# Performance work log

Measured on AMD Instinct MI355X. Metric: run time of the kernel, lower is better.

## Reference

```python
import jax, jax.numpy as jnp
import numpy as np

N_NODES = 50000
N_EDGES = 800000
IN_CH = 128
HID = 128
LAT = 64


def setup_inputs() -> dict:
    key = jax.random.key(0)
    ks = jax.random.split(key, 8)
    s = 1.0 / np.sqrt(IN_CH)
    sh = 1.0 / np.sqrt(HID)
    x = jax.random.normal(ks[0], (N_NODES, IN_CH), dtype=jnp.float32)
    edge_index = jax.random.randint(ks[1], (2, N_EDGES), 0, N_NODES, dtype=jnp.int64)
    return {
        "x": x,
        "edge_index": edge_index,
        "W1": jax.random.normal(ks[2], (IN_CH, HID), dtype=jnp.float32) * s,
        "b1": jnp.zeros((HID,), dtype=jnp.float32),
        "W2": jax.random.normal(ks[3], (HID, HID), dtype=jnp.float32) * sh,
        "b2": jnp.zeros((HID,), dtype=jnp.float32),
        "W_mu": jax.random.normal(ks[4], (HID, LAT), dtype=jnp.float32) * sh,
        "b_mu": jnp.zeros((LAT,), dtype=jnp.float32),
        "W_lv": jax.random.normal(ks[5], (HID, LAT), dtype=jnp.float32) * sh,
        "b_lv": jnp.zeros((LAT,), dtype=jnp.float32),
    }


def _gcn_norm(edge_index, num_nodes):
    # PyG gcn_norm with add_self_loops=True: deg[i] = in-degree(i) + 1
    src, dst = edge_index[0], edge_index[1]
    deg = jax.ops.segment_sum(jnp.ones((edge_index.shape[1],), jnp.float32), dst,
                              num_segments=num_nodes) + 1.0
    dinv = 1.0 / jnp.sqrt(deg)  # deg >= 1, never inf
    edge_norm = dinv[src] * dinv[dst]          # [E]
    self_norm = dinv * dinv                    # [N] norm for self-loop edges
    return src, dst, edge_norm, self_norm


def _gcn_conv(x, W, b, src, dst, edge_norm, self_norm, num_nodes):
    h = x @ W                                           # [N, out]
    msg = h[src] * edge_norm[:, None]                   # [E, out] gather
    agg = jax.ops.segment_sum(msg, dst, num_segments=num_nodes)  # scatter-add
    agg = agg + h * self_norm[:, None]                  # self-loop contribution
    return agg + b


def reference(x, edge_index, W1, b1, W2, b2, W_mu, b_mu, W_lv, b_lv):
    n = x.shape[0]
    src, dst, e_norm, s_norm = _gcn_norm(edge_index, n)
    h = jax.nn.relu(_gcn_conv(x, W1, b1, src, dst, e_norm, s_norm, n))
    h = jax.nn.relu(_gcn_conv(h, W2, b2, src, dst, e_norm, s_norm, n))
    mu = h @ W_mu + b_mu
    logvar = h @ W_lv + b_lv
    return mu, logvar
```

## Files before the change

### kernel.cpp

```cpp
#include <hip/hip_runtime.h>

#define NN 50000
#define NE 800000
#define NSLICE 6250
#define BKT 64

typedef short s8v  __attribute__((ext_vector_type(8)));
typedef float f4v  __attribute__((ext_vector_type(4)));

__device__ __forceinline__ unsigned f2bf(float f) {
    unsigned u = __float_as_uint(f);
    return (u + 0x7fffu + ((u >> 16) & 1u)) >> 16;
}
__device__ __forceinline__ float bf2f_lo(unsigned u) { return __uint_as_float(u << 16); }
__device__ __forceinline__ float bf2f_hi(unsigned u) { return __uint_as_float(u & 0xffff0000u); }

__device__ __forceinline__ s8v pack8(float4 p, float4 q) {
    union { unsigned u[4]; s8v v; } r;
    r.u[0] = (f2bf(p.y) << 16) | f2bf(p.x);
    r.u[1] = (f2bf(p.w) << 16) | f2bf(p.z);
    r.u[2] = (f2bf(q.y) << 16) | f2bf(q.x);
    r.u[3] = (f2bf(q.w) << 16) | f2bf(q.z);
    return r.v;
}

__global__ __launch_bounds__(256) void k_prep(const float* __restrict__ W1, const float* __restrict__ W2,
                                              const float* __restrict__ Wmu, const float* __restrict__ Wlv,
                                              unsigned short* __restrict__ Wt, int* __restrict__ cursor) {
    int b = blockIdx.x;
    if (b < 192) {
        int idx = b * 256 + threadIdx.x;
        int m = idx >> 14, i = idx & 16383;
        int n = i & 127, k = i >> 7;
        float v;
        if (m == 0)      v = W1[k * 128 + n];
        else if (m == 1) v = W2[k * 128 + n];
        else             v = (n < 64) ? Wmu[k * 64 + n] : Wlv[k * 64 + (n - 64)];
        Wt[m * 16384 + n * 128 + k] = (unsigned short)f2bf(v);
    } else {
        int i = (b - 192) * 256 + threadIdx.x;
        if (i < NN) cursor[i] = 0;
    }
}

__global__ __launch_bounds__(256) void k_fg(const float4* __restrict__ x4,
                                            const unsigned short* __restrict__ Wt,
                                            unsigned short* __restrict__ Hb,
                                            const int* __restrict__ src, const int* __restrict__ dst,
                                            int* __restrict__ cursor, int* __restrict__ esrc) {
    int b = blockIdx.x;
    if (b < 782) {
        int wave = threadIdx.x >> 6, lane = threadIdx.x & 63;
        int quad = lane >> 4, l16 = lane & 15;
        int row0 = b * 64 + wave * 16;
        int arow = row0 + l16;
        int arc  = arow < NN ? arow : NN - 1;

        const float4* xq = x4 + (size_t)arc * 32;
        s8v a0 = pack8(xq[ 0 + quad * 2], xq[ 1 + quad * 2]);
        s8v a1 = pack8(xq[ 8 + quad * 2], xq[ 9 + quad * 2]);
        s8v a2 = pack8(xq[16 + quad * 2], xq[17 + quad * 2]);
        s8v a3 = pack8(xq[24 + quad * 2], xq[25 + quad * 2]);

        f4v acc[8];
#pragma unroll
        for (int c = 0; c < 8; ++c) acc[c] = (f4v)0.f;

#pragma unroll
        for (int c = 0; c < 8; ++c) {
            const s8v* wp = (const s8v*)(Wt + (size_t)(c * 16 + l16) * 128);
            acc[c] = __builtin_amdgcn_mfma_f32_16x16x32_bf16(a0, wp[quad],      acc[c], 0, 0, 0);
            acc[c] = __builtin_amdgcn_mfma_f32_16x16x32_bf16(a1, wp[4 + quad],  acc[c], 0, 0, 0);
            acc[c] = __builtin_amdgcn_mfma_f32_16x16x32_bf16(a2, wp[8 + quad],  acc[c], 0, 0, 0);
            acc[c] = __builtin_amdgcn_mfma_f32_16x16x32_bf16(a3, wp[12 + quad], acc[c], 0, 0, 0);
        }

#pragma unroll
        for (int c = 0; c < 8; ++c) {
#pragma unroll
            for (int r = 0; r < 4; ++r) {
                int ro = row0 + quad * 4 + r;
                if (ro < NN) Hb[(size_t)ro * 128 + c * 16 + l16] = (unsigned short)f2bf(acc[c][r]);
            }
        }
    } else {
        int bb = b - 782;
        int xcd = b & 7;
        int e = (bb >> 3) * 256 + threadIdx.x;
        if (e >= NE) return;
        int d = dst[e];
        if (d / NSLICE != xcd) return;
        int s = src[e];
        int p = atomicAdd(&cursor[d], 1);
        if (p < BKT) esrc[(size_t)d * BKT + p] = s;
    }
}

__global__ __launch_bounds__(256) void k_gemm(const unsigned short* __restrict__ Xb,
                                              const unsigned short* __restrict__ Wt,
                                              unsigned short* __restrict__ Cb, int N) {
    int wave = threadIdx.x >> 6, lane = threadIdx.x & 63;
    int quad = lane >> 4, l16 = lane & 15;
    int row0 = blockIdx.x * 64 + wave * 16;
    int arow = row0 + l16;
    int arc  = arow < N ? arow : N - 1;

    const s8v* xp = (const s8v*)(Xb + (size_t)arc * 128);
    s8v a0 = xp[quad], a1 = xp[4 + quad], a2 = xp[8 + quad], a3 = xp[12 + quad];

    f4v acc[8];
#pragma unroll
    for (int c = 0; c < 8; ++c) acc[c] = (f4v)0.f;

#pragma unroll
    for (int c = 0; c < 8; ++c) {
        const s8v* wp = (const s8v*)(Wt + (size_t)(c * 16 + l16) * 128);
        acc[c] = __builtin_amdgcn_mfma_f32_16x16x32_bf16(a0, wp[quad],      acc[c], 0, 0, 0);
        acc[c] = __builtin_amdgcn_mfma_f32_16x16x32_bf16(a1, wp[4 + quad],  acc[c], 0, 0, 0);
        acc[c] = __builtin_amdgcn_mfma_f32_16x16x32_bf16(a2, wp[8 + quad],  acc[c], 0, 0, 0);
        acc[c] = __builtin_amdgcn_mfma_f32_16x16x32_bf16(a3, wp[12 + quad], acc[c], 0, 0, 0);
    }

#pragma unroll
    for (int c = 0; c < 8; ++c) {
#pragma unroll
        for (int r = 0; r < 4; ++r) {
            int ro = row0 + quad * 4 + r;
            if (ro < N) Cb[(size_t)ro * 128 + c * 16 + l16] = (unsigned short)f2bf(acc[c][r]);
        }
    }
}

__global__ __launch_bounds__(256) void k_final(const unsigned short* __restrict__ Xb,
                                               const unsigned short* __restrict__ Wt,
                                               const float* __restrict__ bmu, const float* __restrict__ blv,
                                               float* __restrict__ out, int N) {
    int wave = threadIdx.x >> 6, lane = threadIdx.x & 63;
    int quad = lane >> 4, l16 = lane & 15;
    int row0 = blockIdx.x * 64 + wave * 16;
    int arow = row0 + l16;
    int arc  = arow < N ? arow : N - 1;

    const s8v* xp = (const s8v*)(Xb + (size_t)arc * 128);
    s8v a0 = xp[quad], a1 = xp[4 + quad], a2 = xp[8 + quad], a3 = xp[12 + quad];

    f4v acc[8];
#pragma unroll
    for (int c = 0; c < 8; ++c) acc[c] = (f4v)0.f;

#pragma unroll
    for (int c = 0; c < 8; ++c) {
        const s8v* wp = (const s8v*)(Wt + (size_t)(c * 16 + l16) * 128);
        acc[c] = __builtin_amdgcn_mfma_f32_16x16x32_bf16(a0, wp[quad],      acc[c], 0, 0, 0);
        acc[c] = __builtin_amdgcn_mfma_f32_16x16x32_bf16(a1, wp[4 + quad],  acc[c], 0, 0, 0);
        acc[c] = __builtin_amdgcn_mfma_f32_16x16x32_bf16(a2, wp[8 + quad],  acc[c], 0, 0, 0);
        acc[c] = __builtin_amdgcn_mfma_f32_16x16x32_bf16(a3, wp[12 + quad], acc[c], 0, 0, 0);
    }

#pragma unroll
    for (int c = 0; c < 8; ++c) {
        int col  = c * 16 + l16;
        float bb = (col < 64) ? bmu[col] : blv[col - 64];
#pragma unroll
        for (int r = 0; r < 4; ++r) {
            int ro = row0 + quad * 4 + r;
            if (ro < N) {
                float v = acc[c][r] + bb;
                if (col < 64) out[(size_t)ro * 64 + col] = v;
                else          out[(size_t)NN * 64 + (size_t)ro * 64 + (col - 64)] = v;
            }
        }
    }
}

template<bool FIRST>
__global__ __launch_bounds__(256) void k_agg(const unsigned short* __restrict__ hb,
                                             const int* __restrict__ degc,
                                             const int* __restrict__ esrc,
                                             float* __restrict__ dinv,
                                             const float* __restrict__ b,
                                             unsigned short* __restrict__ outb) {
    int lane = threadIdx.x & 63;
    int n = blockIdx.x * 4 + (threadIdx.x >> 6);
    int d = __builtin_amdgcn_readfirstlane(degc[n]);
    float dn;
    if (FIRST) {
        dn = rsqrtf((float)(d + 1));
        if (lane == 0) dinv[n] = dn;
    } else {
        dn = __uint_as_float(__builtin_amdgcn_readfirstlane(__float_as_uint(dinv[n])));
    }
    const unsigned* h2 = (const unsigned*)hb;
    const int* bk = esrc + (size_t)n * BKT;
    int sv = bk[lane];

    float ax0 = 0.f, ay0 = 0.f, ax1 = 0.f, ay1 = 0.f;
    float ax2 = 0.f, ay2 = 0.f, ax3 = 0.f, ay3 = 0.f;

    {
        unsigned u[24];
        float    w[24];
#pragma unroll
        for (int k = 0; k < 24; ++k) {
            int sraw = __builtin_amdgcn_readlane(sv, k);
            unsigned su = ((unsigned)sraw < (unsigned)NN) ? (unsigned)sraw : 0u;
            float ws;
            if (FIRST) {
                int cs = __builtin_amdgcn_readfirstlane(degc[su]);
                ws = rsqrtf((float)(cs + 1));
            } else {
                ws = __uint_as_float(__builtin_amdgcn_readfirstlane(__float_as_uint(dinv[su])));
            }
            w[k] = (k < d) ? ws * dn : 0.f;
            u[k] = h2[(size_t)su * 64 + lane];
        }
#pragma unroll
        for (int k = 0; k < 24; ++k) {
            float lo = bf2f_lo(u[k]), hi = bf2f_hi(u[k]);
            switch (k & 3) {
                case 0: ax0 += lo * w[k]; ay0 += hi * w[k]; break;
                case 1: ax1 += lo * w[k]; ay1 += hi * w[k]; break;
                case 2: ax2 += lo * w[k]; ay2 += hi * w[k]; break;
                default: ax3 += lo * w[k]; ay3 += hi * w[k]; break;
            }
        }
    }

    for (int e0 = 24; e0 < d; e0 += 8) {
        unsigned u[8];
        float    w[8];
#pragma unroll
        for (int k = 0; k < 8; ++k) {
            int ek  = e0 + k;
            int ekc = ek < (BKT - 1) ? ek : (BKT - 1);
            int sraw = __builtin_amdgcn_readlane(sv, ekc);
            unsigned su = ((unsigned)sraw < (unsigned)NN) ? (unsigned)sraw : 0u;
            float ws;
            if (FIRST) {
                int cs = __builtin_amdgcn_readfirstlane(degc[su]);
                ws = rsqrtf((float)(cs + 1));
            } else {
                ws = __uint_as_float(__builtin_amdgcn_readfirstlane(__float_as_uint(dinv[su])));
            }
            w[k] = (ek < d) ? ws * dn : 0.f;
            u[k] = h2[(size_t)su * 64 + lane];
        }
#pragma unroll
        for (int k = 0; k < 8; ++k) {
            float lo = bf2f_lo(u[k]), hi = bf2f_hi(u[k]);
            switch (k & 3) {
                case 0: ax0 += lo * w[k]; ay0 += hi * w[k]; break;
                case 1: ax1 += lo * w[k]; ay1 += hi * w[k]; break;
                case 2: ax2 += lo * w[k]; ay2 += hi * w[k]; break;
                default: ax3 += lo * w[k]; ay3 += hi * w[k]; break;
            }
        }
    }

    float sn = dn * dn;
    unsigned uh = h2[(size_t)n * 64 + lane];
    float2 bb = ((const float2*)b)[lane];
    float rx = fmaxf((ax0 + ax1) + (ax2 + ax3) + bf2f_lo(uh) * sn + bb.x, 0.f);
    float ry = fmaxf((ay0 + ay1) + (ay2 + ay3) + bf2f_hi(uh) * sn + bb.y, 0.f);
    ((unsigned*)outb)[(size_t)n * 64 + lane] = (f2bf(ry) << 16) | f2bf(rx);
}

extern "C" void kernel_launch(void* const* d_in, const int* in_sizes, int n_in,
                              void* d_out, int out_size, void* d_ws, size_t ws_size,
                              hipStream_t stream) {
    const float* x    = (const float*)d_in[0];
    const int*   eidx = (const int*)d_in[1];
    const float* W1   = (const float*)d_in[2];
    const float* b1   = (const float*)d_in[3];
    const float* W2   = (const float*)d_in[4];
    const float* b2   = (const float*)d_in[5];
    const float* Wmu  = (const float*)d_in[6];
    const float* bmu  = (const float*)d_in[7];
    const float* Wlv  = (const float*)d_in[8];
    const float* blv  = (const float*)d_in[9];
    float* out = (float*)d_out;

    const int* src = eidx;
    const int* dst = eidx + NE;

    float*          ws     = (float*)d_ws;
    int*            cursor = (int*)ws;
    float*          dinv   = ws + 50048;
    int*            esrc   = (int*)(ws + 100096);
    unsigned short* Wt     = (unsigned short*)(ws + 3300096);
    unsigned short* Hb     = (unsigned short*)(ws + 3324672);
    unsigned short* Gb     = (unsigned short*)(ws + 6524672);

    const int gFG = 782 + ((NE + 255) / 256) * 8;
    const int gG  = (NN + 63) / 64;
    const int gA  = NN / 4;

    k_prep<<<388, 256, 0, stream>>>(W1, W2, Wmu, Wlv, Wt, cursor);

    k_fg<<<gFG, 256, 0, stream>>>((const float4*)x, Wt, Hb, src, dst, cursor, esrc);

    k_agg<true><<<gA, 256, 0, stream>>>(Hb, cursor, esrc, dinv, b1, Gb);

    k_gemm<<<gG, 256, 0, stream>>>(Gb, Wt + 16384, Hb, NN);
    k_agg<false><<<gA, 256, 0, stream>>>(Hb, cursor, esrc, dinv, b2, Gb);

    k_final<<<gG, 256, 0, stream>>>(Gb, Wt + 32768, bmu, blv, out, NN);
}
```

Baseline: 270.8 us.

## Fuse aggregation with following GEMM via LDS and vectorize edge bucketing

Merges each aggregation kernel with the next GEMM: every wave aggregates 16 node rows into a swizzled LDS tile, then runs MFMA on it directly, which removes two launches and the bf16 round trip of the aggregated features through global memory. The edge-bucketing part now reads four edges per thread with int4 loads and is placed before the GEMM blocks in the grid. In exchange, each aggregation wave handles 16 rows serially, so fewer independent waves are in flight to hide the random gather latency.

After: 293.8 us. +8.5%, slower.

```diff
diff --git a/kernel.cpp b/kernel.cpp
--- a/kernel.cpp
+++ b/kernel.cpp
@@ -49,10 +49,27 @@
                                             const int* __restrict__ src, const int* __restrict__ dst,
                                             int* __restrict__ cursor, int* __restrict__ esrc) {
     int b = blockIdx.x;
-    if (b < 782) {
+    if (b < 6256) {
+        int xcd = b & 7;
+        int idx = (b >> 3) * 256 + (int)threadIdx.x;
+        if (idx >= NE / 4) return;
+        int4 d4 = ((const int4*)dst)[idx];
+        int4 s4 = ((const int4*)src)[idx];
+        int dv[4] = { d4.x, d4.y, d4.z, d4.w };
+        int sv[4] = { s4.x, s4.y, s4.z, s4.w };
+#pragma unroll
+        for (int k = 0; k < 4; ++k) {
+            int d = dv[k];
+            if (d / NSLICE == xcd) {
+                int p = atomicAdd(&cursor[d], 1);
+                if (p < BKT) esrc[(size_t)d * BKT + p] = sv[k];
+            }
+        }
+    } else {
+        int bg = b - 6256;
         int wave = threadIdx.x >> 6, lane = threadIdx.x & 63;
         int quad = lane >> 4, l16 = lane & 15;
-        int row0 = b * 64 + wave * 16;
+        int row0 = bg * 64 + wave * 16;
         int arow = row0 + l16;
         int arc  = arow < NN ? arow : NN - 1;
 
@@ -83,116 +100,25 @@
                 if (ro < NN) Hb[(size_t)ro * 128 + c * 16 + l16] = (unsigned short)f2bf(acc[c][r]);
             }
         }
-    } else {
-        int bb = b - 782;
-        int xcd = b & 7;
-        int e = (bb >> 3) * 256 + threadIdx.x;
-        if (e >= NE) return;
-        int d = dst[e];
-        if (d / NSLICE != xcd) return;
-        int s = src[e];
-        int p = atomicAdd(&cursor[d], 1);
-        if (p < BKT) esrc[(size_t)d * BKT + p] = s;
-    }
-}
-
-__global__ __launch_bounds__(256) void k_gemm(const unsigned short* __restrict__ Xb,
-                                              const unsigned short* __restrict__ Wt,
-                                              unsigned short* __restrict__ Cb, int N) {
-    int wave = threadIdx.x >> 6, lane = threadIdx.x & 63;
-    int quad = lane >> 4, l16 = lane & 15;
-    int row0 = blockIdx.x * 64 + wave * 16;
-    int arow = row0 + l16;
-    int arc  = arow < N ? arow : N - 1;
-
-    const s8v* xp = (const s8v*)(Xb + (size_t)arc * 128);
-    s8v a0 = xp[quad], a1 = xp[4 + quad], a2 = xp[8 + quad], a3 = xp[12 + quad];
-
-    f4v acc[8];
-#pragma unroll
-    for (int c = 0; c < 8; ++c) acc[c] = (f4v)0.f;
-
-#pragma unroll
-    for (int c = 0; c < 8; ++c) {
-        const s8v* wp = (const s8v*)(Wt + (size_t)(c * 16 + l16) * 128);
-        acc[c] = __builtin_amdgcn_mfma_f32_16x16x32_bf16(a0, wp[quad],      acc[c], 0, 0, 0);
-        acc[c] = __builtin_amdgcn_mfma_f32_16x16x32_bf16(a1, wp[4 + quad],  acc[c], 0, 0, 0);
-        acc[c] = __builtin_amdgcn_mfma_f32_16x16x32_bf16(a2, wp[8 + quad],  acc[c], 0, 0, 0);
-        acc[c] = __builtin_amdgcn_mfma_f32_16x16x32_bf16(a3, wp[12 + quad], acc[c], 0, 0, 0);
-    }
-
-#pragma unroll
-    for (int c = 0; c < 8; ++c) {
-#pragma unroll
-        for (int r = 0; r < 4; ++r) {
-            int ro = row0 + quad * 4 + r;
-            if (ro < N) Cb[(size_t)ro * 128 + c * 16 + l16] = (unsigned short)f2bf(acc[c][r]);
-        }
-    }
-}
-
-__global__ __launch_bounds__(256) void k_final(const unsigned short* __restrict__ Xb,
-                                               const unsigned short* __restrict__ Wt,
-                                               const float* __restrict__ bmu, const float* __restrict__ blv,
-                                               float* __restrict__ out, int N) {
-    int wave = threadIdx.x >> 6, lane = threadIdx.x & 63;
-    int quad = lane >> 4, l16 = lane & 15;
-    int row0 = blockIdx.x * 64 + wave * 16;
-    int arow = row0 + l16;
-    int arc  = arow < N ? arow : N - 1;
-
-    const s8v* xp = (const s8v*)(Xb + (size_t)arc * 128);
-    s8v a0 = xp[quad], a1 = xp[4 + quad], a2 = xp[8 + quad], a3 = xp[12 + quad];
-
-    f4v acc[8];
-#pragma unroll
-    for (int c = 0; c < 8; ++c) acc[c] = (f4v)0.f;
-
-#pragma unroll
-    for (int c = 0; c < 8; ++c) {
-        const s8v* wp = (const s8v*)(Wt + (size_t)(c * 16 + l16) * 128);
-        acc[c] = __builtin_amdgcn_mfma_f32_16x16x32_bf16(a0, wp[quad],      acc[c], 0, 0, 0);
-        acc[c] = __builtin_amdgcn_mfma_f32_16x16x32_bf16(a1, wp[4 + quad],  acc[c], 0, 0, 0);
-        acc[c] = __builtin_amdgcn_mfma_f32_16x16x32_bf16(a2, wp[8 + quad],  acc[c], 0, 0, 0);
-        acc[c] = __builtin_amdgcn_mfma_f32_16x16x32_bf16(a3, wp[12 + quad], acc[c], 0, 0, 0);
-    }
-
-#pragma unroll
-    for (int c = 0; c < 8; ++c) {
-        int col  = c * 16 + l16;
-        float bb = (col < 64) ? bmu[col] : blv[col - 64];
-#pragma unroll
-        for (int r = 0; r < 4; ++r) {
-            int ro = row0 + quad * 4 + r;
-            if (ro < N) {
-                float v = acc[c][r] + bb;
-                if (col < 64) out[(size_t)ro * 64 + col] = v;
-                else          out[(size_t)NN * 64 + (size_t)ro * 64 + (col - 64)] = v;
-            }
-        }
     }
 }
 
 template<bool FIRST>
-__global__ __launch_bounds__(256) void k_agg(const unsigned short* __restrict__ hb,
-                                             const int* __restrict__ degc,
-                                             const int* __restrict__ esrc,
-                                             float* __restrict__ dinv,
-                                             const float* __restrict__ b,
-                                             unsigned short* __restrict__ outb) {
-    int lane = threadIdx.x & 63;
-    int n = blockIdx.x * 4 + (threadIdx.x >> 6);
-    int d = __builtin_amdgcn_readfirstlane(degc[n]);
+__device__ __forceinline__ float2 agg_row(const unsigned* __restrict__ h2,
+                                          const int* __restrict__ degc,
+                                          const int* __restrict__ esrc,
+                                          float* __restrict__ dinv,
+                                          const float* __restrict__ b,
+                                          int nc, int lane) {
+    int d = __builtin_amdgcn_readfirstlane(degc[nc]);
     float dn;
     if (FIRST) {
         dn = rsqrtf((float)(d + 1));
-        if (lane == 0) dinv[n] = dn;
+        if (lane == 0) dinv[nc] = dn;
     } else {
-        dn = __uint_as_float(__builtin_amdgcn_readfirstlane(__float_as_uint(dinv[n])));
-    }
-    const unsigned* h2 = (const unsigned*)hb;
-    const int* bk = esrc + (size_t)n * BKT;
-    int sv = bk[lane];
+        dn = __uint_as_float(__builtin_amdgcn_readfirstlane(__float_as_uint(dinv[nc])));
+    }
+    int sv = esrc[(size_t)nc * BKT + lane];
 
     float ax0 = 0.f, ay0 = 0.f, ax1 = 0.f, ay1 = 0.f;
     float ax2 = 0.f, ay2 = 0.f, ax3 = 0.f, ay3 = 0.f;
@@ -258,11 +184,119 @@
     }
 
     float sn = dn * dn;
-    unsigned uh = h2[(size_t)n * 64 + lane];
+    unsigned uh = h2[(size_t)nc * 64 + lane];
     float2 bb = ((const float2*)b)[lane];
-    float rx = fmaxf((ax0 + ax1) + (ax2 + ax3) + bf2f_lo(uh) * sn + bb.x, 0.f);
-    float ry = fmaxf((ay0 + ay1) + (ay2 + ay3) + bf2f_hi(uh) * sn + bb.y, 0.f);
-    ((unsigned*)outb)[(size_t)n * 64 + lane] = (f2bf(ry) << 16) | f2bf(rx);
+    float2 r;
+    r.x = fmaxf((ax0 + ax1) + (ax2 + ax3) + bf2f_lo(uh) * sn + bb.x, 0.f);
+    r.y = fmaxf((ay0 + ay1) + (ay2 + ay3) + bf2f_hi(uh) * sn + bb.y, 0.f);
+    return r;
+}
+
+__global__ __launch_bounds__(256) void k_ag(const unsigned short* __restrict__ Hb_,
+                                            const int* __restrict__ degc, const int* __restrict__ esrc,
+                                            float* __restrict__ dinv, const float* __restrict__ b1,
+                                            const unsigned short* __restrict__ Wt,
+                                            unsigned short* __restrict__ Cb) {
+    __shared__ __align__(16) unsigned lds[4][16][64];
+    int wave = threadIdx.x >> 6, lane = threadIdx.x & 63;
+    int quad = lane >> 4, l16 = lane & 15;
+    int row0 = blockIdx.x * 64 + wave * 16;
+    const unsigned* h2 = (const unsigned*)Hb_;
+
+#pragma unroll 1
+    for (int j = 0; j < 16; ++j) {
+        int n = row0 + j;
+        int nc = n < NN ? n : NN - 1;
+        float2 r = agg_row<true>(h2, degc, esrc, dinv, b1, nc, lane);
+        lds[wave][j][lane ^ ((j & 7) << 2)] = (f2bf(r.y) << 16) | f2bf(r.x);
+    }
+    __syncthreads();
+
+    const unsigned* rowp = &lds[wave][l16][0];
+    int kx = l16 & 7;
+    s8v a0 = *(const s8v*)(rowp + (( 0 + quad) ^ kx) * 4);
+    s8v a1 = *(const s8v*)(rowp + (( 4 + quad) ^ kx) * 4);
+    s8v a2 = *(const s8v*)(rowp + (( 8 + quad) ^ kx) * 4);
+    s8v a3 = *(const s8v*)(rowp + ((12 + quad) ^ kx) * 4);
+
+    f4v acc[8];
+#pragma unroll
+    for (int c = 0; c < 8; ++c) acc[c] = (f4v)0.f;
+
+#pragma unroll
+    for (int c = 0; c < 8; ++c) {
+        const s8v* wp = (const s8v*)(Wt + (size_t)(c * 16 + l16) * 128);
+        acc[c] = __builtin_amdgcn_mfma_f32_16x16x32_bf16(a0, wp[quad],      acc[c], 0, 0, 0);
+        acc[c] = __builtin_amdgcn_mfma_f32_16x16x32_bf16(a1, wp[4 + quad],  acc[c], 0, 0, 0);
+        acc[c] = __builtin_amdgcn_mfma_f32_16x16x32_bf16(a2, wp[8 + quad],  acc[c], 0, 0, 0);
+        acc[c] = __builtin_amdgcn_mfma_f32_16x16x32_bf16(a3, wp[12 + quad], acc[c], 0, 0, 0);
+    }
+
+#pragma unroll
+    for (int c = 0; c < 8; ++c) {
+#pragma unroll
+        for (int r = 0; r < 4; ++r) {
+            int ro = row0 + quad * 4 + r;
+            if (ro < NN) Cb[(size_t)ro * 128 + c * 16 + l16] = (unsigned short)f2bf(acc[c][r]);
+        }
+    }
+}
+
+__global__ __launch_bounds__(256) void k_af(const unsigned short* __restrict__ Hb_,
+                                            const int* __restrict__ degc, const int* __restrict__ esrc,
+                                            float* __restrict__ dinv, const float* __restrict__ b2,
+                                            const unsigned short* __restrict__ Wt,
+                                            const float* __restrict__ bmu, const float* __restrict__ blv,
+                                            float* __restrict__ out) {
+    __shared__ __align__(16) unsigned lds[4][16][64];
+    int wave = threadIdx.x >> 6, lane = threadIdx.x & 63;
+    int quad = lane >> 4, l16 = lane & 15;
+    int row0 = blockIdx.x * 64 + wave * 16;
+    const unsigned* h2 = (const unsigned*)Hb_;
+
+#pragma unroll 1
+    for (int j = 0; j < 16; ++j) {
+        int n = row0 + j;
+        int nc = n < NN ? n : NN - 1;
+        float2 r = agg_row<false>(h2, degc, esrc, dinv, b2, nc, lane);
+        lds[wave][j][lane ^ ((j & 7) << 2)] = (f2bf(r.y) << 16) | f2bf(r.x);
+    }
+    __syncthreads();
+
+    const unsigned* rowp = &lds[wave][l16][0];
+    int kx = l16 & 7;
+    s8v a0 = *(const s8v*)(rowp + (( 0 + quad) ^ kx) * 4);
+    s8v a1 = *(const s8v*)(rowp + (( 4 + quad) ^ kx) * 4);
+    s8v a2 = *(const s8v*)(rowp + (( 8 + quad) ^ kx) * 4);
+    s8v a3 = *(const s8v*)(rowp + ((12 + quad) ^ kx) * 4);
+
+    f4v acc[8];
+#pragma unroll
+    for (int c = 0; c < 8; ++c) acc[c] = (f4v)0.f;
+
+#pragma unroll
+    for (int c = 0; c < 8; ++c) {
+        const s8v* wp = (const s8v*)(Wt + (size_t)(c * 16 + l16) * 128);
+        acc[c] = __builtin_amdgcn_mfma_f32_16x16x32_bf16(a0, wp[quad],      acc[c], 0, 0, 0);
+        acc[c] = __builtin_amdgcn_mfma_f32_16x16x32_bf16(a1, wp[4 + quad],  acc[c], 0, 0, 0);
+        acc[c] = __builtin_amdgcn_mfma_f32_16x16x32_bf16(a2, wp[8 + quad],  acc[c], 0, 0, 0);
+        acc[c] = __builtin_amdgcn_mfma_f32_16x16x32_bf16(a3, wp[12 + quad], acc[c], 0, 0, 0);
+    }
+
+#pragma unroll
+    for (int c = 0; c < 8; ++c) {
+        int col  = c * 16 + l16;
+        float bb = (col < 64) ? bmu[col] : blv[col - 64];
+#pragma unroll
+        for (int r = 0; r < 4; ++r) {
+            int ro = row0 + quad * 4 + r;
+            if (ro < NN) {
+                float v = acc[c][r] + bb;
+                if (col < 64) out[(size_t)ro * 64 + col] = v;
+                else          out[(size_t)NN * 64 + (size_t)ro * 64 + (col - 64)] = v;
+            }
+        }
+    }
 }
 
 extern "C" void kernel_launch(void* const* d_in, const int* in_sizes, int n_in,
@@ -289,20 +323,16 @@
     int*            esrc   = (int*)(ws + 100096);
     unsigned short* Wt     = (unsigned short*)(ws + 3300096);
     unsigned short* Hb     = (unsigned short*)(ws + 3324672);
-    unsigned short* Gb     = (unsigned short*)(ws + 6524672);
-
-    const int gFG = 782 + ((NE + 255) / 256) * 8;
-    const int gG  = (NN + 63) / 64;
-    const int gA  = NN / 4;
+    unsigned short* Hb2    = (unsigned short*)(ws + 6524672);
+
+    const int gFG = 6256 + 782;
+    const int gA  = 782;
 
     k_prep<<<388, 256, 0, stream>>>(W1, W2, Wmu, Wlv, Wt, cursor);
 
     k_fg<<<gFG, 256, 0, stream>>>((const float4*)x, Wt, Hb, src, dst, cursor, esrc);
 
-    k_agg<true><<<gA, 256, 0, stream>>>(Hb, cursor, esrc, dinv, b1, Gb);
-
-    k_gemm<<<gG, 256, 0, stream>>>(Gb, Wt + 16384, Hb, NN);
-    k_agg<false><<<gA, 256, 0, stream>>>(Hb, cursor, esrc, dinv, b2, Gb);
-
-    k_final<<<gG, 256, 0, stream>>>(Gb, Wt + 32768, bmu, blv, out, NN);
-}
+    k_ag<<<gA, 256, 0, stream>>>(Hb, cursor, esrc, dinv, b1, Wt + 16384, Hb2);
+
+    k_af<<<gA, 256, 0, stream>>>(Hb2, cursor, esrc, dinv, b2, Wt + 32768, bmu, blv, out);
+}
```

## Drop XCD-sliced edge bucketing, put scatter blocks first, use nontemporal stores

Applied to the files above, without the earlier changes.

The edge-bucketing part of the fused GEMM/bucket kernel no longer launches 8 block copies per edge chunk, each filtering edges by destination slice tied to its XCD. It now uses one block per 256 edges with no filtering. Those blocks are scheduled before the GEMM blocks so the atomic scatter starts earlier. The change cuts redundant reads of src/dst and wasted blocks, but loses the L2 locality the per-XCD slicing gave the cursor atomics. All intermediate and final output stores become nontemporal, to avoid polluting cache with streaming writes, though Hb/Gb are re-read by the next kernel.

Result: slower. 294.0 us (+8.6%).

```diff
diff --git a/kernel.cpp b/kernel.cpp
--- a/kernel.cpp
+++ b/kernel.cpp
@@ -2,7 +2,6 @@
 
 #define NN 50000
 #define NE 800000
-#define NSLICE 6250
 #define BKT 64
 
 typedef short s8v  __attribute__((ext_vector_type(8)));
@@ -49,10 +48,17 @@
                                             const int* __restrict__ src, const int* __restrict__ dst,
                                             int* __restrict__ cursor, int* __restrict__ esrc) {
     int b = blockIdx.x;
-    if (b < 782) {
+    if (b < 3125) {
+        int e = b * 256 + (int)threadIdx.x;
+        int d = dst[e];
+        int s = src[e];
+        int p = atomicAdd(&cursor[d], 1);
+        if (p < BKT) esrc[(size_t)d * BKT + p] = s;
+    } else {
+        int bg = b - 3125;
         int wave = threadIdx.x >> 6, lane = threadIdx.x & 63;
         int quad = lane >> 4, l16 = lane & 15;
-        int row0 = b * 64 + wave * 16;
+        int row0 = bg * 64 + wave * 16;
         int arow = row0 + l16;
         int arc  = arow < NN ? arow : NN - 1;
 
@@ -80,19 +86,11 @@
 #pragma unroll
             for (int r = 0; r < 4; ++r) {
                 int ro = row0 + quad * 4 + r;
-                if (ro < NN) Hb[(size_t)ro * 128 + c * 16 + l16] = (unsigned short)f2bf(acc[c][r]);
-            }
-        }
-    } else {
-        int bb = b - 782;
-        int xcd = b & 7;
-        int e = (bb >> 3) * 256 + threadIdx.x;
-        if (e >= NE) return;
-        int d = dst[e];
-        if (d / NSLICE != xcd) return;
-        int s = src[e];
-        int p = atomicAdd(&cursor[d], 1);
-        if (p < BKT) esrc[(size_t)d * BKT + p] = s;
+                if (ro < NN)
+                    __builtin_nontemporal_store((unsigned short)f2bf(acc[c][r]),
+                                                &Hb[(size_t)ro * 128 + c * 16 + l16]);
+            }
+        }
     }
 }
 
@@ -126,7 +124,9 @@
 #pragma unroll
         for (int r = 0; r < 4; ++r) {
             int ro = row0 + quad * 4 + r;
-            if (ro < N) Cb[(size_t)ro * 128 + c * 16 + l16] = (unsigned short)f2bf(acc[c][r]);
+            if (ro < N)
+                __builtin_nontemporal_store((unsigned short)f2bf(acc[c][r]),
+                                            &Cb[(size_t)ro * 128 + c * 16 + l16]);
         }
     }
 }
@@ -166,8 +166,8 @@
             int ro = row0 + quad * 4 + r;
             if (ro < N) {
                 float v = acc[c][r] + bb;
-                if (col < 64) out[(size_t)ro * 64 + col] = v;
-                else          out[(size_t)NN * 64 + (size_t)ro * 64 + (col - 64)] = v;
+                if (col < 64) __builtin_nontemporal_store(v, &out[(size_t)ro * 64 + col]);
+                else          __builtin_nontemporal_store(v, &out[(size_t)NN * 64 + (size_t)ro * 64 + (col - 64)]);
             }
         }
     }
@@ -191,8 +191,7 @@
         dn = __uint_as_float(__builtin_amdgcn_readfirstlane(__float_as_uint(dinv[n])));
     }
     const unsigned* h2 = (const unsigned*)hb;
-    const int* bk = esrc + (size_t)n * BKT;
-    int sv = bk[lane];
+    int sv = esrc[(size_t)n * BKT + lane];
 
     float ax0 = 0.f, ay0 = 0.f, ax1 = 0.f, ay1 = 0.f;
     float ax2 = 0.f, ay2 = 0.f, ax3 = 0.f, ay3 = 0.f;
@@ -262,7 +261,8 @@
     float2 bb = ((const float2*)b)[lane];
     float rx = fmaxf((ax0 + ax1) + (ax2 + ax3) + bf2f_lo(uh) * sn + bb.x, 0.f);
     float ry = fmaxf((ay0 + ay1) + (ay2 + ay3) + bf2f_hi(uh) * sn + bb.y, 0.f);
-    ((unsigned*)outb)[(size_t)n * 64 + lane] = (f2bf(ry) << 16) | f2bf(rx);
+    __builtin_nontemporal_store((f2bf(ry) << 16) | f2bf(rx),
+                                &((unsigned*)outb)[(size_t)n * 64 + lane]);
 }
 
 extern "C" void kernel_launch(void* const* d_in, const int* in_sizes, int n_in,
@@ -291,7 +291,7 @@
     unsigned short* Hb     = (unsigned short*)(ws + 3324672);
     unsigned short* Gb     = (unsigned short*)(ws + 6524672);
 
-    const int gFG = 782 + ((NE + 255) / 256) * 8;
+    const int gFG = 3125 + 782;
     const int gG  = (NN + 63) / 64;
     const int gA  = NN / 4;
 
```
